# Optimization experiments

Hardware: AMD Instinct MI355X
Metric: run time of the kernel (lower is better)

Reference implementation:

```python
import jax, jax.numpy as jnp
import numpy as np

B = 4096        # batch
KD = 64         # koopman_dim
NC = 24         # complex eigenvalue pairs
NR = 16         # real eigenvalues (KD = 2*NC + NR)
DT = 0.01       # delta_t
LC = 2 * NC     # complex net latent/out dim
LR = NR         # real net latent/out dim


def setup_inputs() -> dict:
    key = jax.random.key(0)
    ks = jax.random.split(key, 9)
    def w(k, o, i):
        return jax.random.normal(k, (o, i), dtype=jnp.float32) / np.sqrt(i)
    return {
        "x": jax.random.normal(ks[0], (B, 1, KD), dtype=jnp.float32),
        "Wc1": w(ks[1], LC, KD), "bc1": jnp.zeros((LC,), jnp.float32),
        "Wc2": w(ks[2], LC, LC), "bc2": jnp.zeros((LC,), jnp.float32),
        "Wr1": w(ks[3], LR, KD), "br1": jnp.zeros((LR,), jnp.float32),
        "Wr2": w(ks[4], LR, LR), "br2": jnp.zeros((LR,), jnp.float32),
        "T": 256,
    }


def reference(x, Wc1, bc1, Wc2, bc2, Wr1, br1, Wr2, br2, T):
    # Sequential Koopman rollout. Instead of materializing the [B,KD,KD]
    # block-diagonal K each step, apply the 2x2 rotation*decay blocks and the
    # real decay directly (identical math, no dense matmul).
    dt = jnp.float32(DT)

    def step(y, _):
        # complex parametrization MLP: [B,KD] -> [B,2*NC]
        co = jnp.tanh(y @ Wc1.T + bc1) @ Wc2.T + bc2
        co = co.reshape(-1, NC, 2)
        mu, omega = co[..., 0], co[..., 1]          # [B,NC] each
        scale = jnp.exp(dt * mu)
        c = jnp.cos(dt * omega) * scale             # cos*exp
        s = jnp.sin(dt * omega) * scale             # sin*exp
        yc = y[:, :2 * NC].reshape(-1, NC, 2)       # paired complex coords
        new_c = jnp.stack(
            [c * yc[..., 0] - s * yc[..., 1],
             s * yc[..., 0] + c * yc[..., 1]], axis=-1
        ).reshape(-1, 2 * NC)
        # real parametrization MLP: [B,KD] -> [B,NR]
        re = jnp.tanh(y @ Wr1.T + br1) @ Wr2.T + br2
        new_r = jnp.exp(dt * re) * y[:, 2 * NC:]
        y_new = jnp.concatenate([new_c, new_r], axis=-1)
        return y_new, y_new

    y0 = x[:, 0, :]
    _, Ys = jax.lax.scan(step, y0, None, length=T)  # [T,B,KD]
    return jnp.swapaxes(Ys, 0, 1)                   # [B,T,KD]
```

## Files before the change

### kernel.cpp

```cpp
#include <hip/hip_runtime.h>

#define NB    4096
#define TSTEP 256
#define EPB   16
#define DTC   0.01f

typedef _Float16 h8 __attribute__((ext_vector_type(8)));
typedef _Float16 h4 __attribute__((ext_vector_type(4)));
typedef float    f4 __attribute__((ext_vector_type(4)));

#define KE  0.014426950409f
#define REV 1.59154943e-3f

__device__ __forceinline__ float fast_tanh(float a) {
    float t = fminf(a * 2.885390082f, 126.0f);
    float E = __builtin_amdgcn_exp2f(t);
    return (E - 1.0f) * __builtin_amdgcn_rcpf(E + 1.0f);
}

__device__ __forceinline__ void lds_barrier() {
    asm volatile("s_waitcnt lgkmcnt(0)" ::: "memory");
    __builtin_amdgcn_s_barrier();
    asm volatile("" ::: "memory");
}

#define U16B  2304

__global__ void __launch_bounds__(256)
koopman_kernel(const float* __restrict__ x,
               const float* __restrict__ Wc1, const float* __restrict__ bc1,
               const float* __restrict__ Wc2, const float* __restrict__ bc2,
               const float* __restrict__ Wr1, const float* __restrict__ br1,
               const float* __restrict__ Wr2, const float* __restrict__ br2,
               float* __restrict__ out)
{
    const int tid  = threadIdx.x;
    const int lane = tid & 63;
    const int w    = tid >> 6;
    const int blk  = blockIdx.x;

    __shared__ __align__(16) unsigned char L[U16B * 2];

    const int e = lane & 15;
    const int g = lane >> 4;

    const int fa = 16*w + e;
    h8 a1lo, a1hi, a2lo, a2hi;
    {
        const float* r1 = (fa < 48) ? (Wc1 + fa*64) : (Wr1 + (fa-48)*64);
        #pragma unroll
        for (int i = 0; i < 8; ++i) {
            a1lo[i] = (_Float16)r1[8*g + i];
            a1hi[i] = (_Float16)r1[32 + 8*g + i];
        }
        #pragma unroll
        for (int i = 0; i < 8; ++i) {
            const int k0 = 8*g + i, k1 = k0 + 32;
            float v0, v1;
            if (fa < 48) {
                v0 = (k0 < 48) ? Wc2[fa*48 + k0] : 0.0f;
                v1 = (k1 < 48) ? Wc2[fa*48 + k1] : 0.0f;
            } else {
                v0 = (k0 >= 48) ? Wr2[(fa-48)*16 + (k0-48)] : 0.0f;
                v1 = (k1 >= 48) ? Wr2[(fa-48)*16 + (k1-48)] : 0.0f;
            }
            a2lo[i] = (_Float16)v0;
            a2hi[i] = (_Float16)v1;
        }
    }
    float b1v[4], b2v[4], ys[4];
    #pragma unroll
    for (int r = 0; r < 4; ++r) {
        const int f = 16*w + 4*g + r;
        b1v[r] = (f < 48) ? bc1[f] : br1[f-48];
        b2v[r] = (f < 48) ? bc2[f] : br2[f-48];
        ys[r]  = x[(blk*EPB + e)*64 + f];
    }
    const bool cwave = (w < 3);

    const int rdoff = e*144 + 16*g;
    const int wroff = e*144 + (16*w + 4*g)*2;
    float* gp = out + (size_t)(blk*EPB + e) * (TSTEP*64) + 16*w + 4*g;

    {
        const int row = tid >> 4, col4 = (tid & 15) * 4;
        const f4 xv = *reinterpret_cast<const f4*>(x + (blk*EPB + row)*64 + col4);
        h4 p; p[0]=(_Float16)xv[0]; p[1]=(_Float16)xv[1]; p[2]=(_Float16)xv[2]; p[3]=(_Float16)xv[3];
        *reinterpret_cast<h4*>(L + row*144 + col4*2) = p;
    }
    __syncthreads();

    for (int t = 0; t < TSTEP; ++t) {
        const h8 by0 = *reinterpret_cast<const h8*>(L + rdoff);
        const h8 by1 = *reinterpret_cast<const h8*>(L + rdoff + 64);
        f4 aL = {b1v[0], b1v[1], b1v[2], b1v[3]};
        f4 aH = {0.0f, 0.0f, 0.0f, 0.0f};
        aL = __builtin_amdgcn_mfma_f32_16x16x32_f16(a1lo, by0, aL, 0, 0, 0);
        aH = __builtin_amdgcn_mfma_f32_16x16x32_f16(a1hi, by1, aH, 0, 0, 0);
        const f4 a = aL + aH;
        h4 up;
        up[0]=(_Float16)fast_tanh(a[0]); up[1]=(_Float16)fast_tanh(a[1]);
        up[2]=(_Float16)fast_tanh(a[2]); up[3]=(_Float16)fast_tanh(a[3]);
        *reinterpret_cast<h4*>(L + U16B + wroff) = up;
        lds_barrier();

        const h8 bu0 = *reinterpret_cast<const h8*>(L + U16B + rdoff);
        const h8 bu1 = *reinterpret_cast<const h8*>(L + U16B + rdoff + 64);
        f4 cL = {b2v[0], b2v[1], b2v[2], b2v[3]};
        f4 cH = {0.0f, 0.0f, 0.0f, 0.0f};
        cL = __builtin_amdgcn_mfma_f32_16x16x32_f16(a2lo, bu0, cL, 0, 0, 0);
        cH = __builtin_amdgcn_mfma_f32_16x16x32_f16(a2hi, bu1, cH, 0, 0, 0);
        const f4 c = cL + cH;

        if (cwave) {
            const float sc0 = __builtin_amdgcn_exp2f(KE * c[0]);
            const float sc1 = __builtin_amdgcn_exp2f(KE * c[2]);
            const float s0 = __builtin_amdgcn_sinf(REV * c[1]) * sc0;
            const float c0 = __builtin_amdgcn_cosf(REV * c[1]) * sc0;
            const float s1 = __builtin_amdgcn_sinf(REV * c[3]) * sc1;
            const float c1 = __builtin_amdgcn_cosf(REV * c[3]) * sc1;
            const float n0 = c0*ys[0] - s0*ys[1];
            const float n1 = s0*ys[0] + c0*ys[1];
            const float n2 = c1*ys[2] - s1*ys[3];
            const float n3 = s1*ys[2] + c1*ys[3];
            ys[0]=n0; ys[1]=n1; ys[2]=n2; ys[3]=n3;
        } else {
            ys[0] *= __builtin_amdgcn_exp2f(KE * c[0]);
            ys[1] *= __builtin_amdgcn_exp2f(KE * c[1]);
            ys[2] *= __builtin_amdgcn_exp2f(KE * c[2]);
            ys[3] *= __builtin_amdgcn_exp2f(KE * c[3]);
        }

        h4 yp;
        yp[0]=(_Float16)ys[0]; yp[1]=(_Float16)ys[1]; yp[2]=(_Float16)ys[2]; yp[3]=(_Float16)ys[3];
        *reinterpret_cast<h4*>(L + wroff) = yp;
        f4 yv = {ys[0], ys[1], ys[2], ys[3]};
        *reinterpret_cast<f4*>(gp) = yv;
        gp += 64;
        lds_barrier();
    }
}

extern "C" void kernel_launch(void* const* d_in, const int* in_sizes, int n_in,
                              void* d_out, int out_size, void* d_ws, size_t ws_size,
                              hipStream_t stream) {
    const float* x   = (const float*)d_in[0];
    const float* Wc1 = (const float*)d_in[1];
    const float* bc1 = (const float*)d_in[2];
    const float* Wc2 = (const float*)d_in[3];
    const float* bc2 = (const float*)d_in[4];
    const float* Wr1 = (const float*)d_in[5];
    const float* br1 = (const float*)d_in[6];
    const float* Wr2 = (const float*)d_in[7];
    const float* br2 = (const float*)d_in[8];
    float* out = (float*)d_out;

    koopman_kernel<<<dim3(NB / EPB), dim3(256), 0, stream>>>(
        x, Wc1, bc1, Wc2, bc2, Wr1, br1, Wr2, br2, out);
}
```

Measured before the change: 122.5 us.

## Halve batch rows per block and replace transcendentals with Taylor polynomials

Result: slower. 143.4 us (+17.1%).

```diff
diff --git a/kernel.cpp b/kernel.cpp
--- a/kernel.cpp
+++ b/kernel.cpp
@@ -2,20 +2,20 @@
 
 #define NB    4096
 #define TSTEP 256
-#define EPB   16
+#define EPB   8
 #define DTC   0.01f
 
 typedef _Float16 h8 __attribute__((ext_vector_type(8)));
 typedef _Float16 h4 __attribute__((ext_vector_type(4)));
 typedef float    f4 __attribute__((ext_vector_type(4)));
 
-#define KE  0.014426950409f
-#define REV 1.59154943e-3f
-
 __device__ __forceinline__ float fast_tanh(float a) {
     float t = fminf(a * 2.885390082f, 126.0f);
     float E = __builtin_amdgcn_exp2f(t);
     return (E - 1.0f) * __builtin_amdgcn_rcpf(E + 1.0f);
+}
+__device__ __forceinline__ float texp(float m) {
+    return fmaf(m, fmaf(m, fmaf(m, 1.0f/6.0f, 0.5f), 1.0f), 1.0f);
 }
 
 __device__ __forceinline__ void lds_barrier() {
@@ -41,8 +41,9 @@
 
     __shared__ __align__(16) unsigned char L[U16B * 2];
 
-    const int e = lane & 15;
-    const int g = lane >> 4;
+    const int e  = lane & 15;
+    const int es = e & (EPB - 1);
+    const int g  = lane >> 4;
 
     const int fa = 16*w + e;
     h8 a1lo, a1hi, a2lo, a2hi;
@@ -74,17 +75,18 @@
         const int f = 16*w + 4*g + r;
         b1v[r] = (f < 48) ? bc1[f] : br1[f-48];
         b2v[r] = (f < 48) ? bc2[f] : br2[f-48];
-        ys[r]  = x[(blk*EPB + e)*64 + f];
+        ys[r]  = x[(blk*EPB + es)*64 + f];
     }
     const bool cwave = (w < 3);
 
     const int rdoff = e*144 + 16*g;
     const int wroff = e*144 + (16*w + 4*g)*2;
-    float* gp = out + (size_t)(blk*EPB + e) * (TSTEP*64) + 16*w + 4*g;
+    float* gp = out + (size_t)(blk*EPB + es) * (TSTEP*64) + 16*w + 4*g;
+    const bool do_store = (e < EPB);
 
     {
         const int row = tid >> 4, col4 = (tid & 15) * 4;
-        const f4 xv = *reinterpret_cast<const f4*>(x + (blk*EPB + row)*64 + col4);
+        const f4 xv = *reinterpret_cast<const f4*>(x + (blk*EPB + (row & (EPB-1)))*64 + col4);
         h4 p; p[0]=(_Float16)xv[0]; p[1]=(_Float16)xv[1]; p[2]=(_Float16)xv[2]; p[3]=(_Float16)xv[3];
         *reinterpret_cast<h4*>(L + row*144 + col4*2) = p;
     }
@@ -113,29 +115,35 @@
         const f4 c = cL + cH;
 
         if (cwave) {
-            const float sc0 = __builtin_amdgcn_exp2f(KE * c[0]);
-            const float sc1 = __builtin_amdgcn_exp2f(KE * c[2]);
-            const float s0 = __builtin_amdgcn_sinf(REV * c[1]) * sc0;
-            const float c0 = __builtin_amdgcn_cosf(REV * c[1]) * sc0;
-            const float s1 = __builtin_amdgcn_sinf(REV * c[3]) * sc1;
-            const float c1 = __builtin_amdgcn_cosf(REV * c[3]) * sc1;
-            const float n0 = c0*ys[0] - s0*ys[1];
-            const float n1 = s0*ys[0] + c0*ys[1];
-            const float n2 = c1*ys[2] - s1*ys[3];
-            const float n3 = s1*ys[2] + c1*ys[3];
+            const float m0 = DTC * c[0], x0 = DTC * c[1];
+            const float m1 = DTC * c[2], x1 = DTC * c[3];
+            const float E0 = texp(m0), E1 = texp(m1);
+            const float q0 = x0*x0, q1 = x1*x1;
+            float sp0 = fmaf(q0, 1.0f/120.0f, -1.0f/6.0f); sp0 = fmaf(q0, sp0, 1.0f);
+            float cp0 = fmaf(q0, 1.0f/24.0f,  -0.5f);      cp0 = fmaf(q0, cp0, 1.0f);
+            float sp1 = fmaf(q1, 1.0f/120.0f, -1.0f/6.0f); sp1 = fmaf(q1, sp1, 1.0f);
+            float cp1 = fmaf(q1, 1.0f/24.0f,  -0.5f);      cp1 = fmaf(q1, cp1, 1.0f);
+            const float s0 = E0 * x0 * sp0, c0v = E0 * cp0;
+            const float s1 = E1 * x1 * sp1, c1v = E1 * cp1;
+            const float n0 = c0v*ys[0] - s0*ys[1];
+            const float n1 = s0*ys[0] + c0v*ys[1];
+            const float n2 = c1v*ys[2] - s1*ys[3];
+            const float n3 = s1*ys[2] + c1v*ys[3];
             ys[0]=n0; ys[1]=n1; ys[2]=n2; ys[3]=n3;
         } else {
-            ys[0] *= __builtin_amdgcn_exp2f(KE * c[0]);
-            ys[1] *= __builtin_amdgcn_exp2f(KE * c[1]);
-            ys[2] *= __builtin_amdgcn_exp2f(KE * c[2]);
-            ys[3] *= __builtin_amdgcn_exp2f(KE * c[3]);
+            ys[0] *= texp(DTC * c[0]);
+            ys[1] *= texp(DTC * c[1]);
+            ys[2] *= texp(DTC * c[2]);
+            ys[3] *= texp(DTC * c[3]);
         }
 
         h4 yp;
         yp[0]=(_Float16)ys[0]; yp[1]=(_Float16)ys[1]; yp[2]=(_Float16)ys[2]; yp[3]=(_Float16)ys[3];
         *reinterpret_cast<h4*>(L + wroff) = yp;
-        f4 yv = {ys[0], ys[1], ys[2], ys[3]};
-        *reinterpret_cast<f4*>(gp) = yv;
+        if (do_store) {
+            f4 yv = {ys[0], ys[1], ys[2], ys[3]};
+            *reinterpret_cast<f4*>(gp) = yv;
+        }
         gp += 64;
         lds_barrier();
     }
```
